# Optimization experiments

Hardware: AMD Instinct MI355X
Metric: run time of the kernel (lower is better)

The kernel has to match this reference:

```python
import jax, jax.numpy as jnp
import numpy as np

B, S, HID = 2, 2048, 1024
H, KVH, D = 16, 4, 64
N_REP = H // KVH
SCALE = D ** -0.5
CAP = 50.0


def rotate_half(x):
    x1, x2 = x[..., : D // 2], x[..., D // 2 :]
    return jnp.concatenate((-x2, x1), axis=-1)


def setup_inputs() -> dict:
    key = jax.random.key(0)
    ks = jax.random.split(key, 10)
    X = jax.random.normal(ks[0], (B, S, HID), dtype=jnp.float32)
    # RoPE tables: (B, S, D)
    inv_freq = 1.0 / (10000.0 ** (np.arange(0, D, 2, dtype=np.float32) / D))
    pos = np.arange(S, dtype=np.float32)
    freqs = np.outer(pos, inv_freq)  # (S, D/2)
    emb = np.concatenate([freqs, freqs], axis=-1)  # (S, D)
    cos = jnp.broadcast_to(jnp.asarray(np.cos(emb)), (B, S, D))
    sin = jnp.broadcast_to(jnp.asarray(np.sin(emb)), (B, S, D))
    # causal mask: 1 where key <= query
    mask = jnp.broadcast_to(jnp.tril(jnp.ones((S, S), dtype=jnp.int32)), (B, S, S))
    std = HID ** -0.5
    Wq = jax.random.normal(ks[1], (HID, HID), dtype=jnp.float32) * std
    bq = jnp.zeros((HID,), dtype=jnp.float32)
    Wk = jax.random.normal(ks[2], (KVH * D, HID), dtype=jnp.float32) * std
    bk = jnp.zeros((KVH * D,), dtype=jnp.float32)
    Wv = jax.random.normal(ks[3], (KVH * D, HID), dtype=jnp.float32) * std
    bv = jnp.zeros((KVH * D,), dtype=jnp.float32)
    Wo = jax.random.normal(ks[4], (HID, HID), dtype=jnp.float32) * std
    bo = jnp.zeros((HID,), dtype=jnp.float32)
    return {"X": X, "cos": cos, "sin": sin, "mask": mask,
            "Wq": Wq, "bq": bq, "Wk": Wk, "bk": bk,
            "Wv": Wv, "bv": bv, "Wo": Wo, "bo": bo}


def reference(X, cos, sin, mask, Wq, bq, Wk, bk, Wv, bv, Wo, bo):
    bsz, q_len, _ = X.shape
    q = (X @ Wq.T + bq).reshape(bsz, q_len, H, D).transpose(0, 2, 1, 3)    # (B,H,S,D)
    k = (X @ Wk.T + bk).reshape(bsz, q_len, KVH, D).transpose(0, 2, 1, 3)  # (B,KVH,S,D)
    v = (X @ Wv.T + bv).reshape(bsz, q_len, KVH, D).transpose(0, 2, 1, 3)
    c = cos[:, None, :, :]  # (B,1,S,D)
    s = sin[:, None, :, :]
    q = q * c + rotate_half(q) * s
    k = k * c + rotate_half(k) * s
    k = jnp.repeat(k, N_REP, axis=1)  # GQA expand -> (B,H,S,D)
    v = jnp.repeat(v, N_REP, axis=1)
    scores = jnp.einsum('bhqd,bhkd->bhqk', q, k) * SCALE
    scores = jnp.clip(scores, -CAP, CAP)  # attention cap
    scores = jnp.where(mask[:, None, :, :] == 0, -1e9, scores)
    attn = jax.nn.softmax(scores, axis=-1)  # dropout p=0 -> identity
    ctx = jnp.einsum('bhqk,bhkd->bhqd', attn, v)
    ctx = ctx.transpose(0, 2, 1, 3).reshape(bsz, q_len, H * D)
    out = ctx @ Wo.T + bo
    return (out, attn)
```

## Files before the change

### kernel.cpp

```cpp
#include <hip/hip_runtime.h>
#include <cstdint>
#include <cstddef>

#define S_LEN   2048
#define BATCH   2
#define HID_DIM 1024
#define NHEAD   16
#define NKV     4
#define DHEAD   64
#define SCALE_F 0.125f
#define L2E     1.44269504f
#define QSCALE  (SCALE_F * L2E)
#define CAPL2   (50.0f * L2E)

typedef unsigned short u16;
typedef __attribute__((ext_vector_type(8))) short  short8_t;
typedef __attribute__((ext_vector_type(4))) float  f32x4;
typedef __attribute__((ext_vector_type(4))) u16    u16x4;

static __device__ __forceinline__ u16 f2bf(float f) {
  uint32_t x = __builtin_bit_cast(uint32_t, f);
  x += 0x7fffu + ((x >> 16) & 1u);
  return (u16)(x >> 16);
}

static __device__ __forceinline__ void gload_lds16(const void* g, void* l) {
  __builtin_amdgcn_global_load_lds((const __attribute__((address_space(1))) void*)g,
                                   (__attribute__((address_space(3))) void*)l, 16, 0, 0);
}

static __device__ __forceinline__ float exp2med3(float x) {
  return __builtin_amdgcn_exp2f(__builtin_amdgcn_fmed3f(x, -CAPL2, CAPL2));
}

__global__ void cast_all(const float* __restrict__ X,  u16* __restrict__ xb,
                         const float* __restrict__ Wq, u16* __restrict__ wqb,
                         const float* __restrict__ Wk, u16* __restrict__ wkb,
                         const float* __restrict__ Wv, u16* __restrict__ wvb,
                         const float* __restrict__ Wo, u16* __restrict__ wob) {
  const float* src; u16* dst; int n4;
  switch (blockIdx.y) {
    case 0:  src = X;  dst = xb;  n4 = (BATCH * S_LEN * HID_DIM) / 4; break;
    case 1:  src = Wq; dst = wqb; n4 = (HID_DIM * HID_DIM) / 4;       break;
    case 2:  src = Wk; dst = wkb; n4 = (NKV * DHEAD * HID_DIM) / 4;   break;
    case 3:  src = Wv; dst = wvb; n4 = (NKV * DHEAD * HID_DIM) / 4;   break;
    default: src = Wo; dst = wob; n4 = (HID_DIM * HID_DIM) / 4;       break;
  }
  for (int i = blockIdx.x * 256 + threadIdx.x; i < n4; i += gridDim.x * 256) {
    f32x4 v = ((const f32x4*)src)[i];
    u16x4 o;
    o[0] = f2bf(v[0]); o[1] = f2bf(v[1]); o[2] = f2bf(v[2]); o[3] = f2bf(v[3]);
    ((u16x4*)dst)[i] = o;
  }
}

__global__ __launch_bounds__(256, 4) void gemm_qkv(const u16* __restrict__ Xb,
                                                   const u16* __restrict__ Wqb,
                                                   const u16* __restrict__ Wkb,
                                                   const u16* __restrict__ Wvb,
                                                   const float* __restrict__ bq,
                                                   const float* __restrict__ bk,
                                                   const float* __restrict__ bv,
                                                   const float* __restrict__ cosb,
                                                   const float* __restrict__ sinb,
                                                   u16* __restrict__ qout,
                                                   u16* __restrict__ kout,
                                                   u16* __restrict__ vtout) {
  __shared__ u16 As[64 * 64];
  __shared__ u16 Bs[128 * 64];
  const int tid = threadIdx.x, lane = tid & 63, wid = tid >> 6;
  const int l15 = lane & 15, lg = lane >> 4;
  const int m0 = blockIdx.x * 64, n0 = blockIdx.y * 128;
  const int wm = wid & 1, wn = wid >> 1;
  const int K = HID_DIM;

  const u16* Wp; const float* biasp; int nl, mode;
  if (n0 < 1024)      { Wp = Wqb; biasp = bq; nl = n0;        mode = 0; }
  else if (n0 < 1280) { Wp = Wkb; biasp = bk; nl = n0 - 1024; mode = 1; }
  else                { Wp = Wvb; biasp = bv; nl = n0 - 1280; mode = 2; }

  f32x4 acc[4][2];
  #pragma unroll
  for (int a = 0; a < 4; ++a)
    #pragma unroll
    for (int b2 = 0; b2 < 2; ++b2) acc[a][b2] = (f32x4){0.f, 0.f, 0.f, 0.f};

  const int srow = (lane >> 3), sg = (lane & 7);

  for (int kk = 0; kk < K; kk += 64) {
    __syncthreads();
    #pragma unroll
    for (int i = 0; i < 6; ++i) {
      const int c = wid * 6 + i;
      if (c < 8) {
        const int r = c * 8 + srow;
        const int g = sg ^ (r & 7);
        gload_lds16(Xb + (size_t)(m0 + r) * K + kk + g * 8, As + c * 512);
      } else {
        const int cb = c - 8;
        const int r = cb * 8 + srow;
        const int g = sg ^ (r & 7);
        gload_lds16(Wp + (size_t)(nl + r) * K + kk + g * 8, Bs + cb * 512);
      }
    }
    __syncthreads();
    #pragma unroll
    for (int ks = 0; ks < 2; ++ks) {
      short8_t xa[2], wb[4];
      #pragma unroll
      for (int f = 0; f < 2; ++f) {
        const int rm = wm * 32 + f * 16 + l15;
        xa[f] = *(const short8_t*)(As + rm * 64 + (((ks * 4 + lg) ^ (rm & 7)) * 8));
      }
      #pragma unroll
      for (int f = 0; f < 4; ++f) {
        const int rn = wn * 64 + f * 16 + l15;
        wb[f] = *(const short8_t*)(Bs + rn * 64 + (((ks * 4 + lg) ^ (rn & 7)) * 8));
      }
      if (mode != 2) {
        #pragma unroll
        for (int fn = 0; fn < 4; ++fn)
          #pragma unroll
          for (int fm = 0; fm < 2; ++fm)
            acc[fn][fm] = __builtin_amdgcn_mfma_f32_16x16x32_bf16(wb[fn], xa[fm], acc[fn][fm], 0, 0, 0);
      } else {
        #pragma unroll
        for (int fn = 0; fn < 4; ++fn)
          #pragma unroll
          for (int fm = 0; fm < 2; ++fm)
            acc[fn][fm] = __builtin_amdgcn_mfma_f32_16x16x32_bf16(xa[fm], wb[fn], acc[fn][fm], 0, 0, 0);
      }
    }
  }

  const int m_base = m0 + wm * 32;
  const int nlb = nl + wn * 64;

  if (mode < 2) {
    const int Nout = (mode == 0) ? HID_DIM : (NKV * DHEAD);
    const float qs = (mode == 0) ? QSCALE : 1.0f;
    u16* outb = (mode == 0) ? qout : kout;
    #pragma unroll
    for (int fm = 0; fm < 2; ++fm) {
      const int row = m_base + fm * 16 + l15;
      #pragma unroll
      for (int fn = 0; fn < 2; ++fn) {
        const int dh = fn * 16 + lg * 4;
        const f32x4 c4 = *(const f32x4*)(cosb + (size_t)row * 64 + dh);
        const f32x4 s4 = *(const f32x4*)(sinb + (size_t)row * 64 + dh);
        f32x4 x1 = acc[fn][fm]     + *(const f32x4*)(biasp + nlb + fn * 16 + lg * 4);
        f32x4 x2 = acc[fn + 2][fm] + *(const f32x4*)(biasp + nlb + (fn + 2) * 16 + lg * 4);
        f32x4 o1 = (x1 * c4 - x2 * s4) * qs;
        f32x4 o2 = (x2 * c4 + x1 * s4) * qs;
        u16x4 u1, u2;
        #pragma unroll
        for (int i = 0; i < 4; ++i) { u1[i] = f2bf(o1[i]); u2[i] = f2bf(o2[i]); }
        *(u16x4*)(outb + (size_t)row * Nout + nlb + fn * 16 + lg * 4)       = u1;
        *(u16x4*)(outb + (size_t)row * Nout + nlb + (fn + 2) * 16 + lg * 4) = u2;
      }
    }
  } else {
    #pragma unroll
    for (int fn = 0; fn < 4; ++fn) {
      const int d = nlb + fn * 16 + l15;
      const float bvs = biasp[d];
      #pragma unroll
      for (int fm = 0; fm < 2; ++fm) {
        const int s0 = m_base + fm * 16 + lg * 4;
        const int b_ = s0 >> 11, s_ = s0 & (S_LEN - 1);
        u16x4 o;
        #pragma unroll
        for (int i = 0; i < 4; ++i) o[i] = f2bf(acc[fn][fm][i] + bvs);
        *(u16x4*)(vtout + (size_t)(b_ * 256 + d) * S_LEN + s_) = o;
      }
    }
  }
}

__global__ __launch_bounds__(256, 4) void gemm_out(const u16* __restrict__ A,
                                                   const u16* __restrict__ W,
                                                   const float* __restrict__ bias,
                                                   float* __restrict__ outp) {
  __shared__ u16 As[64 * 64];
  __shared__ u16 Bs[128 * 64];
  const int tid = threadIdx.x, lane = tid & 63, wid = tid >> 6;
  const int l15 = lane & 15, lg = lane >> 4;
  const int m0 = blockIdx.x * 64, n0 = blockIdx.y * 128;
  const int wm = wid & 1, wn = wid >> 1;
  const int K = HID_DIM, N = HID_DIM;

  f32x4 acc[4][2];
  #pragma unroll
  for (int a = 0; a < 4; ++a)
    #pragma unroll
    for (int b2 = 0; b2 < 2; ++b2) acc[a][b2] = (f32x4){0.f, 0.f, 0.f, 0.f};

  const int srow = (lane >> 3), sg = (lane & 7);

  for (int kk = 0; kk < K; kk += 64) {
    __syncthreads();
    #pragma unroll
    for (int i = 0; i < 6; ++i) {
      const int c = wid * 6 + i;
      if (c < 8) {
        const int r = c * 8 + srow;
        const int g = sg ^ (r & 7);
        gload_lds16(A + (size_t)(m0 + r) * K + kk + g * 8, As + c * 512);
      } else {
        const int cb = c - 8;
        const int r = cb * 8 + srow;
        const int g = sg ^ (r & 7);
        gload_lds16(W + (size_t)(n0 + r) * K + kk + g * 8, Bs + cb * 512);
      }
    }
    __syncthreads();
    #pragma unroll
    for (int ks = 0; ks < 2; ++ks) {
      short8_t xa[2], wb[4];
      #pragma unroll
      for (int f = 0; f < 2; ++f) {
        const int rm = wm * 32 + f * 16 + l15;
        xa[f] = *(const short8_t*)(As + rm * 64 + (((ks * 4 + lg) ^ (rm & 7)) * 8));
      }
      #pragma unroll
      for (int f = 0; f < 4; ++f) {
        const int rn = wn * 64 + f * 16 + l15;
        wb[f] = *(const short8_t*)(Bs + rn * 64 + (((ks * 4 + lg) ^ (rn & 7)) * 8));
      }
      #pragma unroll
      for (int fn = 0; fn < 4; ++fn)
        #pragma unroll
        for (int fm = 0; fm < 2; ++fm)
          acc[fn][fm] = __builtin_amdgcn_mfma_f32_16x16x32_bf16(wb[fn], xa[fm], acc[fn][fm], 0, 0, 0);
    }
  }

  const int m_base = m0 + wm * 32, n_base = n0 + wn * 64;
  #pragma unroll
  for (int fn = 0; fn < 4; ++fn) {
    const int col = n_base + fn * 16 + lg * 4;
    const f32x4 bvv = *(const f32x4*)(bias + col);
    #pragma unroll
    for (int fm = 0; fm < 2; ++fm) {
      const int row = m_base + fm * 16 + l15;
      *(f32x4*)(outp + (size_t)row * N + col) = acc[fn][fm] + bvv;
    }
  }
}

__global__ __launch_bounds__(256, 4) void attn_fused(const u16* __restrict__ qb,
                                                     const u16* __restrict__ kb,
                                                     const u16* __restrict__ vtb,
                                                     float* __restrict__ attn,
                                                     u16* __restrict__ ctxb) {
  __shared__ u16 kS[2][64 * 64];
  __shared__ u16 vS[64 * 64];
  __shared__ u16 pS[4][16][72];

  const int tid = threadIdx.x, lane = tid & 63, wid = tid >> 6;
  const int l15 = lane & 15, lg = lane >> 4;
  const int bh = blockIdx.x, b = bh >> 4, h = bh & 15, kvh = h >> 2;
  const int qt = (int)(gridDim.y - 1 - blockIdx.y);
  const int q0 = qt * 64;
  const int NT = qt + 1;
  const int qw = q0 + wid * 16;
  const int qrow = qw + l15;

  const u16* qp = qb + (size_t)(b * S_LEN + qrow) * HID_DIM + h * DHEAD + lg * 8;
  const short8_t qf0 = *(const short8_t*)qp;
  const short8_t qf1 = *(const short8_t*)(qp + 32);

  const u16* kbase  = kb  + (size_t)(b * S_LEN) * (NKV * DHEAD) + kvh * DHEAD;
  const u16* vtbase = vtb + (size_t)(b * NKV + kvh) * DHEAD * S_LEN;

  const int sr8 = wid * 8 + (lane >> 3);
  const int sgr = lane & 7;

  auto stageK = [&](int bi, int kv0) {
    #pragma unroll
    for (int it = 0; it < 2; ++it) {
      const int r = it * 32 + sr8;
      const int g = sgr ^ (r & 7);
      gload_lds16(kbase + (size_t)(kv0 + r) * (NKV * DHEAD) + g * 8,
                  &kS[bi][(it * 32 + wid * 8) * 64]);
    }
  };
  auto stageV = [&](int kv0) {
    #pragma unroll
    for (int it = 0; it < 2; ++it) {
      const int r = it * 32 + sr8;
      const int g = sgr ^ (r & 7);
      gload_lds16(vtbase + (size_t)r * S_LEN + kv0 + g * 8,
                  &vS[(it * 32 + wid * 8) * 64]);
    }
  };

  f32x4 lacc = (f32x4){0.f, 0.f, 0.f, 0.f};
  stageK(0, 0);
  for (int t = 0; t < NT; ++t) {
    const int kv0 = t * 64;
    if (t + 1 < NT) {
      stageK((t + 1) & 1, kv0 + 64);
      asm volatile("s_waitcnt vmcnt(2)" ::: "memory");
    } else {
      asm volatile("s_waitcnt vmcnt(0)" ::: "memory");
    }
    __builtin_amdgcn_s_barrier();
    const u16* ks = kS[t & 1];
    const bool maskc = (kv0 + 63 > qw);
    #pragma unroll
    for (int g16 = 0; g16 < 4; ++g16) {
      const int r = g16 * 16 + l15;
      short8_t ka0 = *(const short8_t*)(ks + r * 64 + ((lg ^ (r & 7)) * 8));
      short8_t ka1 = *(const short8_t*)(ks + r * 64 + (((4 + lg) ^ (r & 7)) * 8));
      f32x4 sacc = (f32x4){0.f, 0.f, 0.f, 0.f};
      sacc = __builtin_amdgcn_mfma_f32_16x16x32_bf16(ka0, qf0, sacc, 0, 0, 0);
      sacc = __builtin_amdgcn_mfma_f32_16x16x32_bf16(ka1, qf1, sacc, 0, 0, 0);
      #pragma unroll
      for (int i = 0; i < 4; ++i) {
        float e = exp2med3(sacc[i]);
        if (maskc) {
          const int kvi = kv0 + g16 * 16 + lg * 4 + i;
          e = (kvi <= qrow) ? e : 0.f;
        }
        lacc[i] += e;
      }
    }
    __builtin_amdgcn_s_barrier();
  }
  float lsum = (lacc[0] + lacc[1]) + (lacc[2] + lacc[3]);
  lsum += __shfl_xor(lsum, 16);
  lsum += __shfl_xor(lsum, 32);
  const float invl = 1.f / lsum;

  float* abase = attn + (size_t)bh * S_LEN * S_LEN;
  float* arow  = abase + (size_t)qrow * S_LEN;
  f32x4 ctx[4];
  #pragma unroll
  for (int dt = 0; dt < 4; ++dt) ctx[dt] = (f32x4){0.f, 0.f, 0.f, 0.f};

  stageK(0, 0);
  asm volatile("s_waitcnt vmcnt(0)" ::: "memory");
  __builtin_amdgcn_s_barrier();

  for (int t = 0; t < NT; ++t) {
    const int kv0 = t * 64;
    stageV(kv0);
    const bool pre = (t + 1 < NT);
    if (pre) stageK((t + 1) & 1, kv0 + 64);

    const u16* ks = kS[t & 1];
    const bool maskc = (kv0 + 63 > qw);
    #pragma unroll
    for (int g16 = 0; g16 < 4; ++g16) {
      const int r = g16 * 16 + l15;
      short8_t ka0 = *(const short8_t*)(ks + r * 64 + ((lg ^ (r & 7)) * 8));
      short8_t ka1 = *(const short8_t*)(ks + r * 64 + (((4 + lg) ^ (r & 7)) * 8));
      f32x4 sacc = (f32x4){0.f, 0.f, 0.f, 0.f};
      sacc = __builtin_amdgcn_mfma_f32_16x16x32_bf16(ka0, qf0, sacc, 0, 0, 0);
      sacc = __builtin_amdgcn_mfma_f32_16x16x32_bf16(ka1, qf1, sacc, 0, 0, 0);
      f32x4 pv; u16x4 pb;
      #pragma unroll
      for (int i = 0; i < 4; ++i) {
        float p = exp2med3(sacc[i]) * invl;
        if (maskc) {
          const int kvi = kv0 + g16 * 16 + lg * 4 + i;
          p = (kvi <= qrow) ? p : 0.f;
        }
        pv[i] = p;
        pb[i] = f2bf(p);
      }
      *(f32x4*)(arow + kv0 + g16 * 16 + lg * 4) = pv;
      *(u16x4*)&pS[wid][l15][g16 * 16 + lg * 4] = pb;
    }

    if (pre) asm volatile("s_waitcnt vmcnt(2)" ::: "memory");
    else     asm volatile("s_waitcnt vmcnt(0)" ::: "memory");
    __builtin_amdgcn_s_barrier();

    short8_t pa0 = *(const short8_t*)&pS[wid][l15][lg * 8];
    short8_t pa1 = *(const short8_t*)&pS[wid][l15][32 + lg * 8];
    #pragma unroll
    for (int dt = 0; dt < 4; ++dt) {
      const int r = dt * 16 + l15;
      short8_t bv0 = *(const short8_t*)(vS + r * 64 + ((lg ^ (r & 7)) * 8));
      short8_t bv1 = *(const short8_t*)(vS + r * 64 + (((4 + lg) ^ (r & 7)) * 8));
      ctx[dt] = __builtin_amdgcn_mfma_f32_16x16x32_bf16(bv0, pa0, ctx[dt], 0, 0, 0);
      ctx[dt] = __builtin_amdgcn_mfma_f32_16x16x32_bf16(bv1, pa1, ctx[dt], 0, 0, 0);
    }

    asm volatile("s_waitcnt vmcnt(0)" ::: "memory");
    __builtin_amdgcn_s_barrier();
  }

  #pragma unroll
  for (int dt = 0; dt < 4; ++dt) {
    u16x4 o;
    #pragma unroll
    for (int i = 0; i < 4; ++i) o[i] = f2bf(ctx[dt][i]);
    *(u16x4*)(ctxb + (size_t)(b * S_LEN + qrow) * HID_DIM + h * DHEAD + dt * 16 + lg * 4) = o;
  }

  const int zc0 = q0 + 64;
  if (zc0 < S_LEN) {
    const f32x4 z = (f32x4){0.f, 0.f, 0.f, 0.f};
    for (int r = wid; r < 64; r += 4) {
      float* rowp = abase + (size_t)(q0 + r) * S_LEN;
      for (int c = zc0 + lane * 4; c < S_LEN; c += 256)
        *(f32x4*)(rowp + c) = z;
    }
  }
}

extern "C" void kernel_launch(void* const* d_in, const int* in_sizes, int n_in,
                              void* d_out, int out_size, void* d_ws, size_t ws_size,
                              hipStream_t stream) {
  (void)in_sizes; (void)n_in; (void)out_size; (void)ws_size;
  const float* X    = (const float*)d_in[0];
  const float* cosb = (const float*)d_in[1];
  const float* sinb = (const float*)d_in[2];
  const float* Wq = (const float*)d_in[4];
  const float* bq = (const float*)d_in[5];
  const float* Wk = (const float*)d_in[6];
  const float* bk = (const float*)d_in[7];
  const float* Wv = (const float*)d_in[8];
  const float* bv = (const float*)d_in[9];
  const float* Wo = (const float*)d_in[10];
  const float* bo = (const float*)d_in[11];

  float* outp  = (float*)d_out;
  float* attnp = outp + (size_t)BATCH * S_LEN * HID_DIM;

  const int M = BATCH * S_LEN;
  u16* ws    = (u16*)d_ws;
  u16* Xb    = ws;
  u16* Wqb   = Xb  + (size_t)M * HID_DIM;
  u16* Wkb   = Wqb + (size_t)HID_DIM * HID_DIM;
  u16* Wvb   = Wkb + (size_t)NKV * DHEAD * HID_DIM;
  u16* Wob   = Wvb + (size_t)NKV * DHEAD * HID_DIM;
  u16* qbuf  = Wob + (size_t)HID_DIM * HID_DIM;
  u16* kbuf  = qbuf + (size_t)M * HID_DIM;
  u16* vtbuf = kbuf + (size_t)M * NKV * DHEAD;
  u16* ctxb  = vtbuf + (size_t)M * NKV * DHEAD;

  cast_all<<<dim3(1024, 5), 256, 0, stream>>>(X, Xb, Wq, Wqb, Wk, Wkb, Wv, Wvb, Wo, Wob);

  gemm_qkv<<<dim3(M / 64, 12), 256, 0, stream>>>(Xb, Wqb, Wkb, Wvb, bq, bk, bv,
                                                 cosb, sinb, qbuf, kbuf, vtbuf);

  attn_fused<<<dim3(BATCH * NHEAD, S_LEN / 64), 256, 0, stream>>>(qbuf, kbuf, vtbuf, attnp, ctxb);

  gemm_out<<<dim3(M / 64, HID_DIM / 128), 256, 0, stream>>>(ctxb, Wob, bo, outp);
}
```

Before: 210.8 us.

## Load K and V fragments directly from global memory instead of LDS staging

Drops the double-buffered LDS staging of K and the LDS staging of V in the fused attention kernel. Each wave now reads its MFMA operands straight from global memory (through cache). This removes the block-wide barriers and vmcnt waits, so waves run independently and can overlap the large attention-probability stores. In exchange, each of the four waves re-reads the same K/V tiles from cache, and global-load latency is no longer hidden by prefetching.

```diff
diff --git a/kernel.cpp b/kernel.cpp
--- a/kernel.cpp
+++ b/kernel.cpp
@@ -253,8 +253,6 @@
                                                      const u16* __restrict__ vtb,
                                                      float* __restrict__ attn,
                                                      u16* __restrict__ ctxb) {
-  __shared__ u16 kS[2][64 * 64];
-  __shared__ u16 vS[64 * 64];
   __shared__ u16 pS[4][16][72];
 
   const int tid = threadIdx.x, lane = tid & 63, wid = tid >> 6;
@@ -273,46 +271,16 @@
   const u16* kbase  = kb  + (size_t)(b * S_LEN) * (NKV * DHEAD) + kvh * DHEAD;
   const u16* vtbase = vtb + (size_t)(b * NKV + kvh) * DHEAD * S_LEN;
 
-  const int sr8 = wid * 8 + (lane >> 3);
-  const int sgr = lane & 7;
-
-  auto stageK = [&](int bi, int kv0) {
-    #pragma unroll
-    for (int it = 0; it < 2; ++it) {
-      const int r = it * 32 + sr8;
-      const int g = sgr ^ (r & 7);
-      gload_lds16(kbase + (size_t)(kv0 + r) * (NKV * DHEAD) + g * 8,
-                  &kS[bi][(it * 32 + wid * 8) * 64]);
-    }
-  };
-  auto stageV = [&](int kv0) {
-    #pragma unroll
-    for (int it = 0; it < 2; ++it) {
-      const int r = it * 32 + sr8;
-      const int g = sgr ^ (r & 7);
-      gload_lds16(vtbase + (size_t)r * S_LEN + kv0 + g * 8,
-                  &vS[(it * 32 + wid * 8) * 64]);
-    }
-  };
-
   f32x4 lacc = (f32x4){0.f, 0.f, 0.f, 0.f};
-  stageK(0, 0);
   for (int t = 0; t < NT; ++t) {
     const int kv0 = t * 64;
-    if (t + 1 < NT) {
-      stageK((t + 1) & 1, kv0 + 64);
-      asm volatile("s_waitcnt vmcnt(2)" ::: "memory");
-    } else {
-      asm volatile("s_waitcnt vmcnt(0)" ::: "memory");
-    }
-    __builtin_amdgcn_s_barrier();
-    const u16* ks = kS[t & 1];
     const bool maskc = (kv0 + 63 > qw);
     #pragma unroll
     for (int g16 = 0; g16 < 4; ++g16) {
       const int r = g16 * 16 + l15;
-      short8_t ka0 = *(const short8_t*)(ks + r * 64 + ((lg ^ (r & 7)) * 8));
-      short8_t ka1 = *(const short8_t*)(ks + r * 64 + (((4 + lg) ^ (r & 7)) * 8));
+      const u16* kp = kbase + (size_t)(kv0 + r) * (NKV * DHEAD) + lg * 8;
+      short8_t ka0 = *(const short8_t*)kp;
+      short8_t ka1 = *(const short8_t*)(kp + 32);
       f32x4 sacc = (f32x4){0.f, 0.f, 0.f, 0.f};
       sacc = __builtin_amdgcn_mfma_f32_16x16x32_bf16(ka0, qf0, sacc, 0, 0, 0);
       sacc = __builtin_amdgcn_mfma_f32_16x16x32_bf16(ka1, qf1, sacc, 0, 0, 0);
@@ -326,7 +294,6 @@
         lacc[i] += e;
       }
     }
-    __builtin_amdgcn_s_barrier();
   }
   float lsum = (lacc[0] + lacc[1]) + (lacc[2] + lacc[3]);
   lsum += __shfl_xor(lsum, 16);
@@ -339,23 +306,15 @@
   #pragma unroll
   for (int dt = 0; dt < 4; ++dt) ctx[dt] = (f32x4){0.f, 0.f, 0.f, 0.f};
 
-  stageK(0, 0);
-  asm volatile("s_waitcnt vmcnt(0)" ::: "memory");
-  __builtin_amdgcn_s_barrier();
-
   for (int t = 0; t < NT; ++t) {
     const int kv0 = t * 64;
-    stageV(kv0);
-    const bool pre = (t + 1 < NT);
-    if (pre) stageK((t + 1) & 1, kv0 + 64);
-
-    const u16* ks = kS[t & 1];
     const bool maskc = (kv0 + 63 > qw);
     #pragma unroll
     for (int g16 = 0; g16 < 4; ++g16) {
       const int r = g16 * 16 + l15;
-      short8_t ka0 = *(const short8_t*)(ks + r * 64 + ((lg ^ (r & 7)) * 8));
-      short8_t ka1 = *(const short8_t*)(ks + r * 64 + (((4 + lg) ^ (r & 7)) * 8));
+      const u16* kp = kbase + (size_t)(kv0 + r) * (NKV * DHEAD) + lg * 8;
+      short8_t ka0 = *(const short8_t*)kp;
+      short8_t ka1 = *(const short8_t*)(kp + 32);
       f32x4 sacc = (f32x4){0.f, 0.f, 0.f, 0.f};
       sacc = __builtin_amdgcn_mfma_f32_16x16x32_bf16(ka0, qf0, sacc, 0, 0, 0);
       sacc = __builtin_amdgcn_mfma_f32_16x16x32_bf16(ka1, qf1, sacc, 0, 0, 0);
@@ -373,24 +332,17 @@
       *(f32x4*)(arow + kv0 + g16 * 16 + lg * 4) = pv;
       *(u16x4*)&pS[wid][l15][g16 * 16 + lg * 4] = pb;
     }
-
-    if (pre) asm volatile("s_waitcnt vmcnt(2)" ::: "memory");
-    else     asm volatile("s_waitcnt vmcnt(0)" ::: "memory");
-    __builtin_amdgcn_s_barrier();
-
     short8_t pa0 = *(const short8_t*)&pS[wid][l15][lg * 8];
     short8_t pa1 = *(const short8_t*)&pS[wid][l15][32 + lg * 8];
     #pragma unroll
     for (int dt = 0; dt < 4; ++dt) {
       const int r = dt * 16 + l15;
-      short8_t bv0 = *(const short8_t*)(vS + r * 64 + ((lg ^ (r & 7)) * 8));
-      short8_t bv1 = *(const short8_t*)(vS + r * 64 + (((4 + lg) ^ (r & 7)) * 8));
+      const u16* vp = vtbase + (size_t)r * S_LEN + kv0 + lg * 8;
+      short8_t bv0 = *(const short8_t*)vp;
+      short8_t bv1 = *(const short8_t*)(vp + 32);
       ctx[dt] = __builtin_amdgcn_mfma_f32_16x16x32_bf16(bv0, pa0, ctx[dt], 0, 0, 0);
       ctx[dt] = __builtin_amdgcn_mfma_f32_16x16x32_bf16(bv1, pa1, ctx[dt], 0, 0, 0);
     }
-
-    asm volatile("s_waitcnt vmcnt(0)" ::: "memory");
-    __builtin_amdgcn_s_barrier();
   }
 
   #pragma unroll
```

After: 312.8 us. +48.4%, slower.
